# Optimization experiments

Hardware: AMD Instinct MI355X
Metric: run time of the kernel (lower is better)

Reference implementation:

```python
import jax, jax.numpy as jnp
import numpy as np

PADDING = 2  # matches init_kwargs; kernel_size = 2*PADDING + 1 -> no circular wrap in roll trick


def setup_inputs() -> dict:
    key = jax.random.key(0)
    k1, k2, k3 = jax.random.split(key, 3)
    x = jax.random.normal(k1, (16, 512, 4096), dtype=jnp.float32)
    weight = jax.random.normal(k2, (512, 512, 5), dtype=jnp.float32)
    bias = jax.random.normal(k3, (512,), dtype=jnp.float32)
    return {"x": x, "weight": weight, "bias": bias}


def reference(x, weight, bias):
    # Original torch module: pad(p,p) -> cat of roll(n-p) copies -> slice -> matmul.
    # Index algebra: out[b,o,t] = sum_{c,n} w[o,c,n] * xpad[b,c, t + 2p - n],
    # which (with kernel_size == 2p+1, so no circular wraparound) is a true
    # convolution, i.e. cross-correlation with the kernel flipped along taps.
    w_flipped = jnp.flip(weight, axis=-1)  # [O, I, K]
    y = jax.lax.conv_general_dilated(
        x, w_flipped,
        window_strides=(1,),
        padding=[(PADDING, PADDING)],
        dimension_numbers=("NCH", "OIH", "NCH"),
    )  # [B, O, T]
    return y + bias[None, :, None]
```

## Files before the change

kernel.cpp:

```cpp
#include <hip/hip_runtime.h>
#include <hip/hip_bf16.h>

typedef __attribute__((ext_vector_type(8))) short short8;
typedef __attribute__((ext_vector_type(4))) float f32x4;

#define B_   16
#define O_   512
#define C_   512
#define T_   4096
#define TP   (T_ + 32)
#define KT   5
#define BM   128
#define BN   128
#define BK   32
#define NCHUNK (C_/BK)

__device__ __forceinline__ void gload_lds16(const void* g, void* l) {
    __builtin_amdgcn_global_load_lds(
        (const __attribute__((address_space(1))) unsigned int*)g,
        (__attribute__((address_space(3))) unsigned int*)l, 16, 0, 0);
}

__global__ void wrepack_kernel(const float* __restrict__ w, unsigned short* __restrict__ wb) {
    int e = blockIdx.x * 256 + threadIdx.x;
    if (e >= KT * O_ * C_) return;
    int n   = e / (O_ * C_);
    int rem = e % (O_ * C_);
    int o   = rem / C_;
    int c   = rem % C_;
    float v = w[((size_t)o * C_ + c) * KT + n];
    __hip_bfloat16 h = __float2bfloat16(v);
    wb[e] = *reinterpret_cast<unsigned short*>(&h);
}

__global__ void padzero_kernel(unsigned short* __restrict__ xt) {
    int i = blockIdx.x * 256 + threadIdx.x;
    if (i >= B_ * 32 * C_) return;
    int b = i / (32 * C_);
    int r = (i / C_) % 32;
    int c = i % C_;
    int tp = (r < 16) ? r : (T_ + r);
    xt[((size_t)b * TP + tp) * C_ + c] = 0;
}

__global__ void xtrans_kernel(const float* __restrict__ x, unsigned short* __restrict__ xt) {
    __shared__ float tile[64][65];
    int b  = blockIdx.z;
    int c0 = blockIdx.y * 64;
    int t0 = blockIdx.x * 64;
    const float* xb = x + ((size_t)b * C_ + c0) * T_ + t0;
#pragma unroll
    for (int p = 0; p < 4; ++p) {
        int idx = p * 256 + threadIdx.x;
        int cl = idx >> 4;
        int tj = (idx & 15) << 2;
        float4 v = *reinterpret_cast<const float4*>(xb + (size_t)cl * T_ + tj);
        tile[cl][tj + 0] = v.x;
        tile[cl][tj + 1] = v.y;
        tile[cl][tj + 2] = v.z;
        tile[cl][tj + 3] = v.w;
    }
    __syncthreads();
    unsigned short* xtb = xt + ((size_t)b * TP + 16 + t0) * C_ + c0;
#pragma unroll
    for (int p = 0; p < 2; ++p) {
        int g  = p * 256 + threadIdx.x;
        int tl = g >> 3;
        int cj = (g & 7) << 3;
        unsigned short tmp[8];
#pragma unroll
        for (int i = 0; i < 8; ++i) {
            __hip_bfloat16 h = __float2bfloat16(tile[cj + i][tl]);
            tmp[i] = *reinterpret_cast<unsigned short*>(&h);
        }
        *reinterpret_cast<short8*>(xtb + (size_t)tl * C_ + cj) =
            *reinterpret_cast<const short8*>(tmp);
    }
}

__global__ __launch_bounds__(256, 3) void conv_gemm_kernel(
        const unsigned short* __restrict__ wb,
        const unsigned short* __restrict__ xt,
        const float* __restrict__ bias,
        float* __restrict__ out) {
    __shared__ unsigned short a_lds[KT * 8 * 512];
    __shared__ unsigned short b_lds[144 * 32];

    int b   = blockIdx.z;
    int o0  = blockIdx.y * BM;
    int t0  = blockIdx.x * BN;
    int tid = threadIdx.x;
    int lane = tid & 63;
    int wid  = tid >> 6;
    int wm = wid >> 1;
    int wn = wid & 1;
    int lr = lane & 15;
    int lg = lane >> 4;

    int bo[KT][4];
#pragma unroll
    for (int n = 0; n < KT; ++n)
#pragma unroll
        for (int ni = 0; ni < 4; ++ni) {
            int row = wn * 64 + ni * 16 + lr + 4 - n;
            bo[n][ni] = row * 32 + ((lg ^ ((row >> 1) & 3)) << 3);
        }

    f32x4 acc[4][4];
#pragma unroll
    for (int mi = 0; mi < 4; ++mi)
#pragma unroll
        for (int ni = 0; ni < 4; ++ni)
            acc[mi][ni] = (f32x4)0.0f;

    const unsigned short* ag = wb + ((size_t)(o0 + lr)) * C_ + lg * 8;
    int c8 = (lane & 3) ^ ((lane >> 3) & 3);
    const unsigned short* bg = xt + ((size_t)b * TP + (t0 + 14 + (lane >> 2))) * C_ + c8 * 8;

    for (int chunk = 0; chunk < NCHUNK; ++chunk) {
        int c0 = chunk * BK;

#pragma unroll
        for (int f = wid; f < 40; f += 4) {
            int n  = f >> 3;
            int rb = f & 7;
            gload_lds16(ag + ((size_t)(n * O_ + rb * 16)) * C_ + c0, &a_lds[f * 512]);
        }
#pragma unroll
        for (int j = wid; j < 9; j += 4) {
            gload_lds16(bg + (size_t)(j * 16) * C_ + c0, &b_lds[j * 512]);
        }
        __syncthreads();

#pragma unroll
        for (int n = 0; n < KT; ++n) {
            short8 af[4], bf[4];
#pragma unroll
            for (int mi = 0; mi < 4; ++mi)
                af[mi] = *reinterpret_cast<const short8*>(
                    &a_lds[(n * 8 + wm * 4 + mi) * 512 + lane * 8]);
#pragma unroll
            for (int ni = 0; ni < 4; ++ni)
                bf[ni] = *reinterpret_cast<const short8*>(&b_lds[bo[n][ni]]);
#pragma unroll
            for (int mi = 0; mi < 4; ++mi)
#pragma unroll
                for (int ni = 0; ni < 4; ++ni)
                    acc[mi][ni] = __builtin_amdgcn_mfma_f32_16x16x32_bf16(
                        af[mi], bf[ni], acc[mi][ni], 0, 0, 0);
        }
        __syncthreads();
    }

#pragma unroll
    for (int mi = 0; mi < 4; ++mi) {
#pragma unroll
        for (int ni = 0; ni < 4; ++ni) {
            int orow = o0 + wm * 64 + mi * 16 + lg * 4;
            int tcol = t0 + wn * 64 + ni * 16 + lr;
#pragma unroll
            for (int r = 0; r < 4; ++r) {
                out[((size_t)b * O_ + orow + r) * T_ + tcol] =
                    acc[mi][ni][r] + bias[orow + r];
            }
        }
    }
}

extern "C" void kernel_launch(void* const* d_in, const int* in_sizes, int n_in,
                              void* d_out, int out_size, void* d_ws, size_t ws_size,
                              hipStream_t stream) {
    const float* x    = (const float*)d_in[0];
    const float* w    = (const float*)d_in[1];
    const float* bias = (const float*)d_in[2];
    float* out        = (float*)d_out;

    unsigned short* wb  = (unsigned short*)d_ws;
    unsigned short* xtp = wb + (size_t)KT * O_ * C_;

    padzero_kernel<<<(B_ * 32 * C_ + 255) / 256, 256, 0, stream>>>(xtp);
    wrepack_kernel<<<(KT * O_ * C_ + 255) / 256, 256, 0, stream>>>(w, wb);
    xtrans_kernel<<<dim3(T_ / 64, C_ / 64, B_), 256, 0, stream>>>(x, xtp);
    conv_gemm_kernel<<<dim3(T_ / BN, O_ / BM, B_), 256, 0, stream>>>(wb, xtp, bias, out);
}
```

Baseline: 232.0 us.

## Double-buffer LDS, widen tile to 256 columns with 8 waves, swizzle block order

The conv GEMM now uses a 128x256 output tile computed by 8 waves (512 threads), which halves how often the five-tap weight slab is reloaded per output column. A/B tiles are double-buffered in LDS so the next channel chunk's global-to-LDS loads are in flight during the current chunk's MFMAs. The launch becomes a flat 1024-block grid with an XCD-style swizzle. MFMA sections are wrapped in s_setprio. LDS usage roughly doubles and occupancy drops to one block per CU.

```diff
diff --git a/kernel.cpp b/kernel.cpp
--- a/kernel.cpp
+++ b/kernel.cpp
@@ -11,7 +11,7 @@
 #define TP   (T_ + 32)
 #define KT   5
 #define BM   128
-#define BN   128
+#define BN   256
 #define BK   32
 #define NCHUNK (C_/BK)
 
@@ -78,24 +78,29 @@
     }
 }
 
-__global__ __launch_bounds__(256, 3) void conv_gemm_kernel(
+__global__ __launch_bounds__(512, 1) void conv_gemm_kernel(
         const unsigned short* __restrict__ wb,
         const unsigned short* __restrict__ xt,
         const float* __restrict__ bias,
         float* __restrict__ out) {
-    __shared__ unsigned short a_lds[KT * 8 * 512];
-    __shared__ unsigned short b_lds[144 * 32];
+    __shared__ unsigned short a_lds[2][KT * 8 * 512];
+    __shared__ unsigned short b_lds[2][272 * 32];
 
-    int b   = blockIdx.z;
-    int o0  = blockIdx.y * BM;
-    int t0  = blockIdx.x * BN;
-    int tid = threadIdx.x;
+    int bid = blockIdx.x;
+    int swz = (bid & 7) * 128 + (bid >> 3);
+    int o_t = swz & 3;
+    int t_t = (swz >> 2) & 15;
+    int b   = swz >> 6;
+    int o0  = o_t * BM;
+    int t0  = t_t * BN;
+
+    int tid  = threadIdx.x;
     int lane = tid & 63;
     int wid  = tid >> 6;
-    int wm = wid >> 1;
-    int wn = wid & 1;
-    int lr = lane & 15;
-    int lg = lane >> 4;
+    int wm   = wid >> 2;
+    int wn   = wid & 3;
+    int lr   = lane & 15;
+    int lg   = lane >> 4;
 
     int bo[KT][4];
 #pragma unroll
@@ -113,24 +118,31 @@
         for (int ni = 0; ni < 4; ++ni)
             acc[mi][ni] = (f32x4)0.0f;
 
-    const unsigned short* ag = wb + ((size_t)(o0 + lr)) * C_ + lg * 8;
+    const unsigned short* ag = wb + (size_t)(o0 + lr) * C_ + lg * 8;
     int c8 = (lane & 3) ^ ((lane >> 3) & 3);
     const unsigned short* bg = xt + ((size_t)b * TP + (t0 + 14 + (lane >> 2))) * C_ + c8 * 8;
 
+#pragma unroll
+    for (int f = wid; f < 40; f += 8)
+        gload_lds16(ag + (size_t)((f >> 3) * O_ + (f & 7) * 16) * C_, &a_lds[0][f * 512]);
+#pragma unroll
+    for (int j = wid; j < 17; j += 8)
+        gload_lds16(bg + (size_t)(j * 16) * C_, &b_lds[0][j * 512]);
+    __syncthreads();
+
     for (int chunk = 0; chunk < NCHUNK; ++chunk) {
-        int c0 = chunk * BK;
+        int cur = chunk & 1;
 
+        if (chunk + 1 < NCHUNK) {
+            int c0 = (chunk + 1) * BK;
 #pragma unroll
-        for (int f = wid; f < 40; f += 4) {
-            int n  = f >> 3;
-            int rb = f & 7;
-            gload_lds16(ag + ((size_t)(n * O_ + rb * 16)) * C_ + c0, &a_lds[f * 512]);
+            for (int f = wid; f < 40; f += 8)
+                gload_lds16(ag + (size_t)((f >> 3) * O_ + (f & 7) * 16) * C_ + c0,
+                            &a_lds[cur ^ 1][f * 512]);
+#pragma unroll
+            for (int j = wid; j < 17; j += 8)
+                gload_lds16(bg + (size_t)(j * 16) * C_ + c0, &b_lds[cur ^ 1][j * 512]);
         }
-#pragma unroll
-        for (int j = wid; j < 9; j += 4) {
-            gload_lds16(bg + (size_t)(j * 16) * C_ + c0, &b_lds[j * 512]);
-        }
-        __syncthreads();
 
 #pragma unroll
         for (int n = 0; n < KT; ++n) {
@@ -138,16 +150,18 @@
 #pragma unroll
             for (int mi = 0; mi < 4; ++mi)
                 af[mi] = *reinterpret_cast<const short8*>(
-                    &a_lds[(n * 8 + wm * 4 + mi) * 512 + lane * 8]);
+                    &a_lds[cur][(n * 8 + wm * 4 + mi) * 512 + lane * 8]);
 #pragma unroll
             for (int ni = 0; ni < 4; ++ni)
-                bf[ni] = *reinterpret_cast<const short8*>(&b_lds[bo[n][ni]]);
+                bf[ni] = *reinterpret_cast<const short8*>(&b_lds[cur][bo[n][ni]]);
+            __builtin_amdgcn_s_setprio(1);
 #pragma unroll
             for (int mi = 0; mi < 4; ++mi)
 #pragma unroll
                 for (int ni = 0; ni < 4; ++ni)
                     acc[mi][ni] = __builtin_amdgcn_mfma_f32_16x16x32_bf16(
                         af[mi], bf[ni], acc[mi][ni], 0, 0, 0);
+            __builtin_amdgcn_s_setprio(0);
         }
         __syncthreads();
     }
@@ -181,5 +195,5 @@
     padzero_kernel<<<(B_ * 32 * C_ + 255) / 256, 256, 0, stream>>>(xtp);
     wrepack_kernel<<<(KT * O_ * C_ + 255) / 256, 256, 0, stream>>>(w, wb);
     xtrans_kernel<<<dim3(T_ / 64, C_ / 64, B_), 256, 0, stream>>>(x, xtp);
-    conv_gemm_kernel<<<dim3(T_ / BN, O_ / BM, B_), 256, 0, stream>>>(wb, xtp, bias, out);
+    conv_gemm_kernel<<<1024, 512, 0, stream>>>(wb, xtp, bias, out);
 }
```

New measurement: 234.0 us. Within noise of the previous version (+0.9%).
